# Kernel optimization log

Hardware: AMD Instinct MI355X
Metric: run time of the kernel (lower is better)

The kernel has to match this reference:

```python
import jax, jax.numpy as jnp
import numpy as np

B, S, HID = 2, 4096, 1024
NH, HD = 16, 64
R = 2  # dilation_rate


def setup_inputs() -> dict:
    key = jax.random.key(0)
    ks = jax.random.split(key, 6)
    sc = 0.02
    return {
        "hidden_states": jax.random.normal(ks[0], (B, S, HID), jnp.float32),
        "Wq": jax.random.normal(ks[1], (HID, HID), jnp.float32) * sc,
        "Wk": jax.random.normal(ks[2], (HID, HID), jnp.float32) * sc,
        "Wv": jax.random.normal(ks[3], (HID, HID), jnp.float32) * sc,
        "Wo": jax.random.normal(ks[4], (HID, HID), jnp.float32) * sc,
        "bo": jnp.zeros((HID,), jnp.float32),
    }


def reference(hidden_states, Wq, Wk, Wv, Wo, bo):
    bsz, q_len, _ = hidden_states.shape
    # projections (torch Linear: y = x @ W.T)
    q = jnp.einsum('bsh,oh->bso', hidden_states, Wq).reshape(bsz, q_len, NH, HD).transpose(0, 2, 1, 3)
    k = jnp.einsum('bsh,oh->bso', hidden_states, Wk).reshape(bsz, q_len, NH, HD).transpose(0, 2, 1, 3)
    v = jnp.einsum('bsh,oh->bso', hidden_states, Wv).reshape(bsz, q_len, NH, HD).transpose(0, 2, 1, 3)
    # strided dilation gather (indices 0, R, 2R, ...)
    q = q[:, :, ::R, :]
    k = k[:, :, ::R, :]
    v = v[:, :, ::R, :]
    sd = q.shape[2]  # dilated length
    # SDPA with is_causal=True over the dilated subsequence
    scores = jnp.einsum('bhqd,bhkd->bhqk', q, k) / np.sqrt(HD).astype(np.float32)
    causal = jnp.tril(jnp.ones((sd, sd), bool))
    scores = jnp.where(causal, scores, jnp.finfo(scores.dtype).min)
    probs = jax.nn.softmax(scores, axis=-1)
    attn = jnp.einsum('bhqk,bhkd->bhqd', probs, v)  # [B, H, sd, HD]
    attn = attn.transpose(0, 2, 1, 3).reshape(bsz, sd, HID)
    # scatter back into zero-initialized full-length tensor
    full = jnp.zeros((bsz, q_len, HID), attn.dtype).at[:, ::R, :].set(attn)
    return jnp.einsum('bsh,oh->bso', full, Wo) + bo
```

## Files before the change

kernel.cpp:

```cpp
#include <hip/hip_runtime.h>
#include <cstdint>

typedef unsigned short u16;
typedef unsigned int u32;
typedef __attribute__((ext_vector_type(8))) short short8;
typedef __attribute__((ext_vector_type(4))) float f32x4;
typedef __attribute__((ext_vector_type(4))) unsigned short u16x4;
typedef __attribute__((ext_vector_type(4))) u32 u32x4;
typedef __attribute__((ext_vector_type(2))) u32 u32x2;

#define S_ 4096
#define SD 2048

__device__ __forceinline__ u16 f2bf(float f) {
  union { float f; u32 u; } v; v.f = f;
  u32 r = v.u + 0x7fffu + ((v.u >> 16) & 1u);
  return (u16)(r >> 16);
}
#if __has_builtin(__builtin_amdgcn_cvt_pk_bf16_f32)
__device__ __forceinline__ u32 pkbf(float a, float b) {
  auto r = __builtin_amdgcn_cvt_pk_bf16_f32(a, b);
  u32 o; __builtin_memcpy(&o, &r, 4); return o;
}
#else
__device__ __forceinline__ u32 pkbf(float a, float b) {
  union { float f; u32 u; } ua, ub; ua.f = a; ub.f = b;
  return __builtin_amdgcn_perm(ub.u + 0x8000u, ua.u + 0x8000u, 0x07060302u);
}
#endif
__device__ __forceinline__ f32x4 mfma16(short8 a, short8 b, f32x4 c) {
  return __builtin_amdgcn_mfma_f32_16x16x32_bf16(a, b, c, 0, 0, 0);
}
__device__ __forceinline__ void async16(const void* g, void* l) {
  __builtin_amdgcn_global_load_lds((__attribute__((address_space(1))) void*)g,
                                   (__attribute__((address_space(3))) void*)l,
                                   16, 0, 0);
}

__global__ __launch_bounds__(256) void cast_all(const float* __restrict__ hs,
                                                const float* __restrict__ Wq,
                                                const float* __restrict__ Wk,
                                                const float* __restrict__ Wv,
                                                const float* __restrict__ Wo,
                                                u16* __restrict__ dstW,
                                                u16* __restrict__ dstX) {
  int bid = blockIdx.x;
  if (bid < 4096) {
    int gid = bid * 256 + threadIdx.x;
    int wsel = gid >> 18;
    int off  = (gid & 262143) * 4;
    const float* src = (wsel == 0) ? Wq : (wsel == 1) ? Wk : (wsel == 2) ? Wv : Wo;
    float scl = (wsel == 0) ? 0.18033688f : 1.0f;
    f32x4 v = *(const f32x4*)(src + off);
    u16x4 o; o.x = f2bf(v.x * scl); o.y = f2bf(v.y * scl);
    o.z = f2bf(v.z * scl); o.w = f2bf(v.w * scl);
    *(u16x4*)(dstW + (size_t)wsel * 1048576 + off) = o;
  } else {
    int gid = (bid - 4096) * 256 + threadIdx.x;
    int e = gid * 4;
    int m = e >> 10, col = e & 1023;
    int b = m >> 11, sm = m & 2047;
    const float* src = hs + ((size_t)(b * S_ + 2 * sm) << 10) + col;
    f32x4 v = *(const f32x4*)src;
    u16x4 o; o.x = f2bf(v.x); o.y = f2bf(v.y); o.z = f2bf(v.z); o.w = f2bf(v.w);
    *(u16x4*)(dstX + ((size_t)m << 10) + col) = o;
  }
}

__device__ __forceinline__ void gemm_body128(const u16* __restrict__ A,
                                             const u16* __restrict__ B,
                                             u16* __restrict__ C, int N,
                                             int bm, int bn, char* lA, char* lB) {
  const int tid = threadIdx.x, lane = tid & 63, w = tid >> 6;
  const int quad = lane >> 4, l15 = lane & 15;
  const int wm = (w & 1) * 64, wn = (w >> 1) * 64;
  f32x4 acc[4][4] = {};

  auto stage = [&](int buf, int k0) {
#pragma unroll
    for (int i = 0; i < 2; i++) {
      int p = i * 256 + tid;
      int row = p >> 2, cp = p & 3;
      int c = cp ^ ((row ^ (row >> 2)) & 3);
      async16(A + (size_t)(bm + row) * 1024 + k0 + c * 8,
              lA + buf * 8192 + i * 4096 + w * 1024);
      async16(B + (size_t)(bn + row) * 1024 + k0 + c * 8,
              lB + buf * 8192 + i * 4096 + w * 1024);
    }
  };

  stage(0, 0);
#pragma unroll 1
  for (int kt = 0; kt < 32; kt++) {
    __syncthreads();
    if (kt + 1 < 32) stage((kt + 1) & 1, (kt + 1) * 32);
    const char* A_ = lA + (kt & 1) * 8192;
    const char* B_ = lB + (kt & 1) * 8192;
    short8 af[4], bf[4];
#pragma unroll
    for (int mi = 0; mi < 4; mi++) {
      int row = wm + mi * 16 + l15;
      af[mi] = *(const short8*)(A_ + (row * 4 + (quad ^ ((row ^ (row >> 2)) & 3))) * 16);
    }
#pragma unroll
    for (int ni = 0; ni < 4; ni++) {
      int row = wn + ni * 16 + l15;
      bf[ni] = *(const short8*)(B_ + (row * 4 + (quad ^ ((row ^ (row >> 2)) & 3))) * 16);
    }
#pragma unroll
    for (int mi = 0; mi < 4; mi++)
#pragma unroll
      for (int ni = 0; ni < 4; ni++)
        acc[mi][ni] = mfma16(af[mi], bf[ni], acc[mi][ni]);
  }
#pragma unroll
  for (int mi = 0; mi < 4; mi++)
#pragma unroll
    for (int ni = 0; ni < 4; ni++) {
      int m0 = bm + wm + mi * 16 + quad * 4;
      int n = bn + wn + ni * 16 + l15;
#pragma unroll
      for (int r = 0; r < 4; r++)
        C[(size_t)(m0 + r) * N + n] = f2bf(acc[mi][ni][r]);
    }
}

__global__ __launch_bounds__(256) void qkv_gemm(const u16* __restrict__ X,
                                                const u16* __restrict__ Wbf,
                                                u16* __restrict__ QK,
                                                u16* __restrict__ Vt) {
  __shared__ __align__(16) char lA[16384];
  __shared__ __align__(16) char lB[16384];
  int bid = blockIdx.x;
  if (bid < 512) {
    gemm_body128(X, Wbf, QK, 2048, (bid >> 4) * 128, (bid & 15) * 128, lA, lB);
  } else {
    int b2 = bid - 512;
    gemm_body128(Wbf + 2 * 1048576, X, Vt, 4096, (b2 >> 5) * 128, (b2 & 31) * 128, lA, lB);
  }
}

__global__ __launch_bounds__(256) void oproj(const u16* __restrict__ A,
                                             const u16* __restrict__ B,
                                             const float* __restrict__ bo,
                                             float* __restrict__ out) {
  __shared__ __align__(16) char lA[8192];
  __shared__ __align__(16) char lB[16384];
  const int tid = threadIdx.x, lane = tid & 63, w = tid >> 6;
  const int quad = lane >> 4, l15 = lane & 15;
  const int bm = blockIdx.y * 64, bn = blockIdx.x * 128;
  const int wm = (w & 1) * 32, wn = (w >> 1) * 64;
  f32x4 acc[2][4] = {};

  auto stage = [&](int buf, int k0) {
    {
      int row = tid >> 2, cp = tid & 3;
      int c = cp ^ ((row ^ (row >> 2)) & 3);
      async16(A + (size_t)(bm + row) * 1024 + k0 + c * 8, lA + buf * 4096 + w * 1024);
    }
#pragma unroll
    for (int i = 0; i < 2; i++) {
      int p = i * 256 + tid;
      int row = p >> 2, cp = p & 3;
      int c = cp ^ ((row ^ (row >> 2)) & 3);
      async16(B + (size_t)(bn + row) * 1024 + k0 + c * 8, lB + buf * 8192 + i * 4096 + w * 1024);
    }
  };

  stage(0, 0);
#pragma unroll 1
  for (int kt = 0; kt < 32; kt++) {
    __syncthreads();
    if (kt + 1 < 32) stage((kt + 1) & 1, (kt + 1) * 32);
    const char* A_ = lA + (kt & 1) * 4096;
    const char* B_ = lB + (kt & 1) * 8192;
    short8 af[2], bf[4];
#pragma unroll
    for (int mi = 0; mi < 2; mi++) {
      int row = wm + mi * 16 + l15;
      af[mi] = *(const short8*)(A_ + (row * 4 + (quad ^ ((row ^ (row >> 2)) & 3))) * 16);
    }
#pragma unroll
    for (int ni = 0; ni < 4; ni++) {
      int row = wn + ni * 16 + l15;
      bf[ni] = *(const short8*)(B_ + (row * 4 + (quad ^ ((row ^ (row >> 2)) & 3))) * 16);
    }
#pragma unroll
    for (int mi = 0; mi < 2; mi++)
#pragma unroll
      for (int ni = 0; ni < 4; ni++)
        acc[mi][ni] = mfma16(af[mi], bf[ni], acc[mi][ni]);
  }
#pragma unroll
  for (int mi = 0; mi < 2; mi++)
#pragma unroll
    for (int ni = 0; ni < 4; ni++) {
      int n = bn + wn + ni * 16 + l15;
      float bias = bo[n];
#pragma unroll
      for (int r = 0; r < 4; r++) {
        int m = bm + wm + mi * 16 + quad * 4 + r;
        int bb = m >> 11, sm = m & 2047;
        size_t grow = ((size_t)(bb * S_ + 2 * sm)) << 10;
        out[grow + n] = acc[mi][ni][r] + bias;
        out[grow + 1024 + n] = bias;
      }
    }
}

__global__ __launch_bounds__(128, 3) void attn7(const u16* __restrict__ QK,
                                                const u16* __restrict__ Vt,
                                                u16* __restrict__ O) {
  __shared__ __align__(16) char lK[2][8192];
  __shared__ __align__(16) char lV[2][8192];
  const int tid = threadIdx.x, lane = tid & 63, w = tid >> 6;
  const int quad = lane >> 4, l15 = lane & 15;
  const int h = blockIdx.x, b = blockIdx.y;
  const int qt = 31 - (int)blockIdx.z;
  const int qb = qt * 64 + w * 32;

  short8 qf[2][2];
#pragma unroll
  for (int n = 0; n < 2; n++) {
    const u16* qp = QK + (size_t)(b * SD + qb + n * 16 + l15) * 2048 + h * 64 + quad * 8;
    qf[n][0] = *(const short8*)qp;
    qf[n][1] = *(const short8*)(qp + 32);
  }

  auto stageK = [&](int buf, int kb) {
#pragma unroll
    for (int i = 0; i < 4; i++) {
      int p = (w * 4 + i) * 64 + lane;
      int row = p >> 3, c = (p & 7) ^ (row & 7);
      async16(QK + (size_t)(b * SD + kb + row) * 2048 + 1024 + h * 64 + c * 8,
              lK[buf] + (w * 4 + i) * 1024);
    }
  };

  const int vd = tid >> 1, g = tid & 1;
  const u16* vgbase = Vt + (size_t)(h * 64 + vd) * 4096 + b * SD;
  const int vs = vd & 7;
  int aw[8];
#pragma unroll
  for (int j = 0; j < 4; j++) {
    int G = g + 2 * j;
#pragma unroll
    for (int s = 0; s < 2; s++) {
      int q = 2 * G + s;
      aw[j * 2 + s] = vd * 128 + (((q & 3) + 4 * (q >> 3)) ^ vs) * 16 + ((q >> 2) & 1) * 8;
    }
  }

  u32x4 nv[4];
  auto loadV = [&](int kb) {
#pragma unroll
    for (int j = 0; j < 4; j++)
      nv[j] = *(const u32x4*)(vgbase + kb + (g + 2 * j) * 8);
  };
  auto writeV = [&](int buf) {
    char* Vn = lV[buf];
#pragma unroll
    for (int j = 0; j < 4; j++) {
      *(u32x2*)(Vn + aw[j * 2])     = u32x2{nv[j].x, nv[j].y};
      *(u32x2*)(Vn + aw[j * 2 + 1]) = u32x2{nv[j].z, nv[j].w};
    }
  };

  f32x4 oacc[2][4] = {};
  f32x4 l4v[2] = {};
  const f32x4 zf = {};

  stageK(0, 0);
  loadV(0);
  writeV(0);

#pragma unroll 1
  for (int kt = 0; kt <= qt; kt++) {
    __syncthreads();
    if (kt + 1 <= qt) {
      stageK((kt + 1) & 1, (kt + 1) * 64);
      loadV((kt + 1) * 64);
    }
    const char* K_ = lK[kt & 1];
    const char* V_ = lV[kt & 1];
    const bool last = (kt == qt);

    u32 pw[2][8];
#pragma unroll
    for (int m = 0; m < 4; m++) {
      int key = m * 16 + l15;
      short8 kf0 = *(const short8*)(K_ + (key * 8 + (quad ^ (key & 7))) * 16);
      short8 kf1 = *(const short8*)(K_ + (key * 8 + ((4 + quad) ^ (key & 7))) * 16);
#pragma unroll
      for (int n = 0; n < 2; n++) {
        f32x4 a = mfma16(kf0, qf[n][0], zf);
        a = mfma16(kf1, qf[n][1], a);
        if (last) {
          int qrel = w * 32 + n * 16 + l15;
#pragma unroll
          for (int r = 0; r < 4; r++)
            if (m * 16 + quad * 4 + r > qrel) a[r] = -1e30f;
        }
        f32x4 p;
#pragma unroll
        for (int r = 0; r < 4; r++) p[r] = exp2f(a[r]);
        l4v[n] += p;
        pw[n][m * 2]     = pkbf(p[0], p[1]);
        pw[n][m * 2 + 1] = pkbf(p[2], p[3]);
      }
    }
    short8 pf[2][2];
#pragma unroll
    for (int n = 0; n < 2; n++) {
      __builtin_memcpy(&pf[n][0], &pw[n][0], 16);
      __builtin_memcpy(&pf[n][1], &pw[n][4], 16);
    }

#pragma unroll
    for (int m = 0; m < 4; m++) {
      int dr = m * 16 + l15;
      short8 vf0 = *(const short8*)(V_ + (dr * 128 + ((quad     ^ (dr & 7)) * 16)));
      short8 vf1 = *(const short8*)(V_ + (dr * 128 + (((4+quad) ^ (dr & 7)) * 16)));
#pragma unroll
      for (int n = 0; n < 2; n++) {
        oacc[n][m] = mfma16(vf0, pf[n][0], oacc[n][m]);
        oacc[n][m] = mfma16(vf1, pf[n][1], oacc[n][m]);
      }
    }
    if (kt + 1 <= qt) writeV((kt + 1) & 1);
  }

#pragma unroll
  for (int n = 0; n < 2; n++) {
    float l = (l4v[n][0] + l4v[n][1]) + (l4v[n][2] + l4v[n][3]);
    l += __shfl_xor(l, 16, 64);
    l += __shfl_xor(l, 32, 64);
    float inv = 1.0f / l;
    u16* op = O + (size_t)(b * SD + qb + n * 16 + l15) * 1024 + h * 64;
#pragma unroll
    for (int m = 0; m < 4; m++) {
      u16x4 ov;
#pragma unroll
      for (int r = 0; r < 4; r++) ov[r] = f2bf(oacc[n][m][r] * inv);
      *(u16x4*)(op + m * 16 + quad * 4) = ov;
    }
  }
}

extern "C" void kernel_launch(void* const* d_in, const int* in_sizes, int n_in,
                              void* d_out, int out_size, void* d_ws, size_t ws_size,
                              hipStream_t stream) {
  (void)in_sizes; (void)n_in; (void)out_size; (void)ws_size;
  const float* hs = (const float*)d_in[0];
  const float* Wq = (const float*)d_in[1];
  const float* Wk = (const float*)d_in[2];
  const float* Wv = (const float*)d_in[3];
  const float* Wo = (const float*)d_in[4];
  const float* bo = (const float*)d_in[5];
  float* out = (float*)d_out;
  char* ws = (char*)d_ws;

  u16* Xbf = (u16*)ws;
  u16* Wbf = (u16*)(ws + (8u << 20));
  u16* QKb = (u16*)(ws + (16u << 20));
  u16* Vtb = (u16*)(ws + (32u << 20));
  u16* Ob  = (u16*)(ws + (40u << 20));

  cast_all<<<8192, 256, 0, stream>>>(hs, Wq, Wk, Wv, Wo, Wbf, Xbf);
  qkv_gemm<<<768, 256, 0, stream>>>(Xbf, Wbf, QKb, Vtb);
  attn7<<<dim3(16, 2, 32), 128, 0, stream>>>(QKb, Vtb, Ob);
  oproj<<<dim3(8, 64), 256, 0, stream>>>(Ob, Wbf + 3 * 1048576, bo, out);
}
```

Measured before the change: 211.1 us.

## Store K and V in MFMA fragment order and read attention operands directly from global

The QKV GEMM epilogue now writes K and V into per-(batch, head, 64-key tile) blocks laid out in MFMA fragment order, so each lane's operand is one contiguous 16-byte load. The attention kernel drops LDS staging, double buffering and barriers entirely. It runs one 64-thread wave per 32-query chunk and reads K/V fragments straight from global memory, doubling the grid. This removes LDS traffic and sync overhead but gives up K/V reuse across waves, so it relies on L2 cache hits and loses async prefetch overlap.

```diff
diff --git a/kernel.cpp b/kernel.cpp
--- a/kernel.cpp
+++ b/kernel.cpp
@@ -6,8 +6,6 @@
 typedef __attribute__((ext_vector_type(8))) short short8;
 typedef __attribute__((ext_vector_type(4))) float f32x4;
 typedef __attribute__((ext_vector_type(4))) unsigned short u16x4;
-typedef __attribute__((ext_vector_type(4))) u32 u32x4;
-typedef __attribute__((ext_vector_type(2))) u32 u32x2;
 
 #define S_ 4096
 #define SD 2048
@@ -67,10 +65,11 @@
   }
 }
 
-__device__ __forceinline__ void gemm_body128(const u16* __restrict__ A,
-                                             const u16* __restrict__ B,
-                                             u16* __restrict__ C, int N,
-                                             int bm, int bn, char* lA, char* lB) {
+template<int MODE>
+__device__ __forceinline__ void gemm_body128_t(const u16* __restrict__ A,
+                                               const u16* __restrict__ B,
+                                               u16* __restrict__ C,
+                                               int bm, int bn, char* lA, char* lB) {
   const int tid = threadIdx.x, lane = tid & 63, w = tid >> 6;
   const int quad = lane >> 4, l15 = lane & 15;
   const int wm = (w & 1) * 64, wn = (w >> 1) * 64;
@@ -113,30 +112,55 @@
       for (int ni = 0; ni < 4; ni++)
         acc[mi][ni] = mfma16(af[mi], bf[ni], acc[mi][ni]);
   }
+
 #pragma unroll
   for (int mi = 0; mi < 4; mi++)
 #pragma unroll
     for (int ni = 0; ni < 4; ni++) {
       int m0 = bm + wm + mi * 16 + quad * 4;
       int n = bn + wn + ni * 16 + l15;
-#pragma unroll
-      for (int r = 0; r < 4; r++)
-        C[(size_t)(m0 + r) * N + n] = f2bf(acc[mi][ni][r]);
+      size_t base;
+      if (MODE == 0) {
+        base = (size_t)m0 * 1024 + n;
+      } else if (MODE == 1) {
+        int bb = m0 >> 11, t = m0 & 2047, kb = t >> 6, key0 = t & 63;
+        int d = n - 1024;
+        int hh = d >> 6, dd = d & 63, ch = dd >> 3, e = dd & 7;
+        base = ((size_t)(((bb * 16 + hh) * 32 + kb)) << 12)
+             + (key0 >> 4) * 1024 + (ch >> 2) * 512 + (ch & 3) * 128
+             + (key0 & 15) * 8 + e;
+      } else {
+        int hh = m0 >> 6, d0 = m0 & 63;
+        int bb = n >> 11, t = n & 2047, kb = t >> 6, kk = t & 63;
+        int kh = (kk & 32) | (((kk >> 2) & 3) << 3) | (((kk >> 4) & 1) << 2) | (kk & 3);
+        int ch = kh >> 3, e = kh & 7;
+        base = ((size_t)(((bb * 16 + hh) * 32 + kb)) << 12)
+             + (d0 >> 4) * 1024 + (ch >> 2) * 512 + (ch & 3) * 128
+             + (d0 & 15) * 8 + e;
+      }
+#pragma unroll
+      for (int r = 0; r < 4; r++) {
+        size_t off = (MODE == 0) ? base + (size_t)r * 1024 : base + (size_t)r * 8;
+        C[off] = f2bf(acc[mi][ni][r]);
+      }
     }
 }
 
 __global__ __launch_bounds__(256) void qkv_gemm(const u16* __restrict__ X,
                                                 const u16* __restrict__ Wbf,
-                                                u16* __restrict__ QK,
-                                                u16* __restrict__ Vt) {
+                                                u16* __restrict__ Qb,
+                                                u16* __restrict__ Kp,
+                                                u16* __restrict__ Vp) {
   __shared__ __align__(16) char lA[16384];
   __shared__ __align__(16) char lB[16384];
   int bid = blockIdx.x;
   if (bid < 512) {
-    gemm_body128(X, Wbf, QK, 2048, (bid >> 4) * 128, (bid & 15) * 128, lA, lB);
+    int bm = (bid >> 4) * 128, bn = (bid & 15) * 128;
+    if (bn < 1024) gemm_body128_t<0>(X, Wbf, Qb, bm, bn, lA, lB);
+    else           gemm_body128_t<1>(X, Wbf, Kp, bm, bn, lA, lB);
   } else {
     int b2 = bid - 512;
-    gemm_body128(Wbf + 2 * 1048576, X, Vt, 4096, (b2 >> 5) * 128, (b2 & 31) * 128, lA, lB);
+    gemm_body128_t<2>(Wbf + 2 * 1048576, X, Vp, (b2 >> 5) * 128, (b2 & 31) * 128, lA, lB);
   }
 }
 
@@ -208,98 +232,50 @@
     }
 }
 
-__global__ __launch_bounds__(128, 3) void attn7(const u16* __restrict__ QK,
-                                                const u16* __restrict__ Vt,
-                                                u16* __restrict__ O) {
-  __shared__ __align__(16) char lK[2][8192];
-  __shared__ __align__(16) char lV[2][8192];
-  const int tid = threadIdx.x, lane = tid & 63, w = tid >> 6;
-  const int quad = lane >> 4, l15 = lane & 15;
+__global__ __launch_bounds__(64) void attn10(const u16* __restrict__ Qb,
+                                             const u16* __restrict__ Kp,
+                                             const u16* __restrict__ Vp,
+                                             u16* __restrict__ O) {
+  const int lane = threadIdx.x & 63, quad = lane >> 4, l15 = lane & 15;
   const int h = blockIdx.x, b = blockIdx.y;
-  const int qt = 31 - (int)blockIdx.z;
-  const int qb = qt * 64 + w * 32;
+  const int c = 63 - (int)blockIdx.z;
+  const int qb = c * 32;
+  const int nt = (c >> 1) + 1;
 
   short8 qf[2][2];
 #pragma unroll
   for (int n = 0; n < 2; n++) {
-    const u16* qp = QK + (size_t)(b * SD + qb + n * 16 + l15) * 2048 + h * 64 + quad * 8;
+    const u16* qp = Qb + (size_t)(b * SD + qb + n * 16 + l15) * 1024 + h * 64 + quad * 8;
     qf[n][0] = *(const short8*)qp;
     qf[n][1] = *(const short8*)(qp + 32);
   }
 
-  auto stageK = [&](int buf, int kb) {
-#pragma unroll
-    for (int i = 0; i < 4; i++) {
-      int p = (w * 4 + i) * 64 + lane;
-      int row = p >> 3, c = (p & 7) ^ (row & 7);
-      async16(QK + (size_t)(b * SD + kb + row) * 2048 + 1024 + h * 64 + c * 8,
-              lK[buf] + (w * 4 + i) * 1024);
-    }
-  };
-
-  const int vd = tid >> 1, g = tid & 1;
-  const u16* vgbase = Vt + (size_t)(h * 64 + vd) * 4096 + b * SD;
-  const int vs = vd & 7;
-  int aw[8];
-#pragma unroll
-  for (int j = 0; j < 4; j++) {
-    int G = g + 2 * j;
-#pragma unroll
-    for (int s = 0; s < 2; s++) {
-      int q = 2 * G + s;
-      aw[j * 2 + s] = vd * 128 + (((q & 3) + 4 * (q >> 3)) ^ vs) * 16 + ((q >> 2) & 1) * 8;
-    }
-  }
-
-  u32x4 nv[4];
-  auto loadV = [&](int kb) {
-#pragma unroll
-    for (int j = 0; j < 4; j++)
-      nv[j] = *(const u32x4*)(vgbase + kb + (g + 2 * j) * 8);
-  };
-  auto writeV = [&](int buf) {
-    char* Vn = lV[buf];
-#pragma unroll
-    for (int j = 0; j < 4; j++) {
-      *(u32x2*)(Vn + aw[j * 2])     = u32x2{nv[j].x, nv[j].y};
-      *(u32x2*)(Vn + aw[j * 2 + 1]) = u32x2{nv[j].z, nv[j].w};
-    }
-  };
-
+  const size_t bh = (size_t)(b * 16 + h) * 32;
   f32x4 oacc[2][4] = {};
   f32x4 l4v[2] = {};
   const f32x4 zf = {};
 
-  stageK(0, 0);
-  loadV(0);
-  writeV(0);
-
 #pragma unroll 1
-  for (int kt = 0; kt <= qt; kt++) {
-    __syncthreads();
-    if (kt + 1 <= qt) {
-      stageK((kt + 1) & 1, (kt + 1) * 64);
-      loadV((kt + 1) * 64);
-    }
-    const char* K_ = lK[kt & 1];
-    const char* V_ = lV[kt & 1];
-    const bool last = (kt == qt);
+  for (int kt = 0; kt < nt; kt++) {
+    const u16* K_ = Kp + ((bh + kt) << 12);
+    const u16* V_ = Vp + ((bh + kt) << 12);
+    const bool last = (kt == nt - 1);
 
     u32 pw[2][8];
 #pragma unroll
     for (int m = 0; m < 4; m++) {
-      int key = m * 16 + l15;
-      short8 kf0 = *(const short8*)(K_ + (key * 8 + (quad ^ (key & 7))) * 16);
-      short8 kf1 = *(const short8*)(K_ + (key * 8 + ((4 + quad) ^ (key & 7))) * 16);
+      short8 kf0 = *(const short8*)(K_ + m * 1024 + lane * 8);
+      short8 kf1 = *(const short8*)(K_ + m * 1024 + 512 + lane * 8);
 #pragma unroll
       for (int n = 0; n < 2; n++) {
         f32x4 a = mfma16(kf0, qf[n][0], zf);
         a = mfma16(kf1, qf[n][1], a);
         if (last) {
-          int qrel = w * 32 + n * 16 + l15;
+          int qr = (c & 1) * 32 + n * 16 + l15;
+          int kd = m * 16 + quad * 4;
 #pragma unroll
           for (int r = 0; r < 4; r++)
-            if (m * 16 + quad * 4 + r > qrel) a[r] = -1e30f;
+            if (kd + r > qr) a[r] = -1e30f;
         }
         f32x4 p;
 #pragma unroll
@@ -318,16 +294,14 @@
 
 #pragma unroll
     for (int m = 0; m < 4; m++) {
-      int dr = m * 16 + l15;
-      short8 vf0 = *(const short8*)(V_ + (dr * 128 + ((quad     ^ (dr & 7)) * 16)));
-      short8 vf1 = *(const short8*)(V_ + (dr * 128 + (((4+quad) ^ (dr & 7)) * 16)));
+      short8 vf0 = *(const short8*)(V_ + m * 1024 + lane * 8);
+      short8 vf1 = *(const short8*)(V_ + m * 1024 + 512 + lane * 8);
 #pragma unroll
       for (int n = 0; n < 2; n++) {
         oacc[n][m] = mfma16(vf0, pf[n][0], oacc[n][m]);
         oacc[n][m] = mfma16(vf1, pf[n][1], oacc[n][m]);
       }
     }
-    if (kt + 1 <= qt) writeV((kt + 1) & 1);
   }
 
 #pragma unroll
@@ -362,12 +336,13 @@
 
   u16* Xbf = (u16*)ws;
   u16* Wbf = (u16*)(ws + (8u << 20));
-  u16* QKb = (u16*)(ws + (16u << 20));
-  u16* Vtb = (u16*)(ws + (32u << 20));
+  u16* Qb  = (u16*)(ws + (16u << 20));
+  u16* Kp  = (u16*)(ws + (24u << 20));
+  u16* Vp  = (u16*)(ws + (32u << 20));
   u16* Ob  = (u16*)(ws + (40u << 20));
 
   cast_all<<<8192, 256, 0, stream>>>(hs, Wq, Wk, Wv, Wo, Wbf, Xbf);
-  qkv_gemm<<<768, 256, 0, stream>>>(Xbf, Wbf, QKb, Vtb);
-  attn7<<<dim3(16, 2, 32), 128, 0, stream>>>(QKb, Vtb, Ob);
+  qkv_gemm<<<768, 256, 0, stream>>>(Xbf, Wbf, Qb, Kp, Vp);
+  attn10<<<dim3(16, 2, 64), 64, 0, stream>>>(Qb, Kp, Vp, Ob);
   oproj<<<dim3(8, 64), 256, 0, stream>>>(Ob, Wbf + 3 * 1048576, bo, out);
 }
```

New measurement: 248.5 us. +17.7%, slower.
